# Performance work log

Hardware: AMD Instinct MI355X
Metric: run time of the kernel (lower is better)

## Reference

```python
import jax, jax.numpy as jnp
import numpy as np

# H2RConfig constants
KERNEL = 3
MAX_ROUTES = 1000
STRIDE = 4.0
MIN_SIZE = 32.0
MAX_SIZE = 512.0
SCORE_POWER = 2.0
UNC_WEIGHT = 0.35


def setup_inputs() -> dict:
    key = jax.random.key(0)
    k1, k2, k3 = jax.random.split(key, 3)
    shape = (32, 1, 512, 512)  # [B, 1, H, W] heatmaps at stride 4
    return {
        "route_logits": jax.random.normal(k1, shape, jnp.float32),
        "scale_logits": jax.random.normal(k2, shape, jnp.float32),
        "uncertainty_logits": jax.random.normal(k3, shape, jnp.float32),
        "image_h": 2048,
        "image_w": 2048,
    }


def reference(route_logits, scale_logits, uncertainty_logits, image_h, image_w):
    # score map: sigmoid^power, modulated by uncertainty (use_route_uncertainty=True)
    score = jnp.power(jax.nn.sigmoid(route_logits), SCORE_POWER)
    score = score * (1.0 - UNC_WEIGHT * jax.nn.sigmoid(uncertainty_logits))

    # local-max NMS: 3x3 max pool, stride 1, SAME padding (torch pads with -inf)
    pooled = jax.lax.reduce_window(
        score, -jnp.inf, jax.lax.max,
        window_dimensions=(1, 1, KERNEL, KERNEL),
        window_strides=(1, 1, 1, 1),
        padding="SAME",
    )
    peak_mask = score == pooled
    filtered = jnp.where(peak_mask, score, -1.0)

    B = score.shape[0]
    Wd = score.shape[3]
    flat = filtered.reshape(B, -1)                 # [B, H*W]
    values, indices = jax.lax.top_k(flat, MAX_ROUTES)  # [B, K]
    valid = values > 0.0                            # torch drops these; we mask/pad

    ys = indices // Wd
    xs = indices % Wd
    cx = (xs.astype(jnp.float32) + 0.5) * STRIDE
    cy = (ys.astype(jnp.float32) + 0.5) * STRIDE

    # gather scale / uncertainty at peak locations
    sc = jnp.take_along_axis(scale_logits.reshape(B, -1), indices, axis=1)
    un = jax.nn.sigmoid(jnp.take_along_axis(uncertainty_logits.reshape(B, -1), indices, axis=1))

    side = MIN_SIZE + jax.nn.sigmoid(sc) * (MAX_SIZE - MIN_SIZE)
    side = side * (1.0 + 0.25 * un)
    half = side * 0.5

    iw = float(image_w)
    ih = float(image_h)
    x1 = jnp.clip(cx - half, 0.0, iw - 1.0)
    y1 = jnp.clip(cy - half, 0.0, ih - 1.0)
    x2 = jnp.clip(cx + half, 1.0, iw)
    y2 = jnp.clip(cy + half, 1.0, ih)

    bcol = jnp.broadcast_to(jnp.arange(B, dtype=jnp.float32)[:, None], values.shape)
    rois = jnp.stack([bcol, x1, y1, x2, y2], axis=-1)  # [B, K, 5]

    # padded (fixed-shape) equivalent of torch's variable-length concat
    rois = jnp.where(valid[..., None], rois, 0.0)
    scores = jnp.where(valid, values, 0.0)
    return rois, scores, valid
```

## Files before the change

### kernel.cpp

```cpp
#include <hip/hip_runtime.h>
#include <hip/hip_bf16.h>
#include <math.h>


#define B_   32
#define H_   512
#define W_   512
#define HW_  (H_ * W_)
#define K_   1000
#define ROWS_ 16
#define THR_  512
#define PBUF_ 2048
#define PCAP_ 32768
#define CAND_ 2048

__device__ __forceinline__ float np_expf(float x) {
#pragma clang fp contract(off)
    const float log2e = 1.44269504088896341f;
    float z = x * log2e;
    float m = rintf(z);
    float r = fmaf(m, -0.693359375f, x);
    r = fmaf(m, 2.12194440e-4f, r);
    float r2 = r * r;
    float p = fmaf(1.9875691500e-4f, r, 1.3981999507e-3f);
    p = fmaf(p, r, 8.3334519073e-3f);
    p = fmaf(p, r, 4.1665795894e-2f);
    p = fmaf(p, r, 1.6666665459e-1f);
    p = fmaf(p, r, 5.0000001201e-1f);
    p = fmaf(p, r2, r);
    p = p + 1.0f;
    int mi = (int)m;
    float sc = __int_as_float((127 + mi) << 23);
    return p * sc;
}

__device__ __forceinline__ float sigmoid_np(float x) {
#pragma clang fp contract(off)
    float e = np_expf(-x);
    float d = 1.0f + e;
    return 1.0f / d;
}

__device__ __forceinline__ float score_ref(float r, float u) {
#pragma clang fp contract(off)
    float s  = sigmoid_np(r);
    float s2 = s * s;
    float su = sigmoid_np(u);
    float t  = 0.35f * su;
    float m  = 1.0f - t;
    return s2 * m;
}

__device__ __forceinline__ float sigmoid_fast(float x) {
    return 1.0f / (1.0f + __expf(-x));
}

__global__ __launch_bounds__(THR_, 4) void fused_peak_kernel(
    const float* __restrict__ route, const float* __restrict__ unc,
    unsigned long long* __restrict__ plist, int* __restrict__ peak_cnt)
{
    __shared__ float sm[ROWS_ + 2][W_];
    __shared__ unsigned long long pbuf[PBUF_];
    __shared__ int lcnt, gbase;

    const int tid   = threadIdx.x;
    const int strip = blockIdx.x;
    const int b     = blockIdx.y;
    const int r0    = strip * ROWS_;
    if (tid == 0) lcnt = 0;

    const float4* rb4 = (const float4*)(route + (size_t)b * HW_);
    const float4* ub4 = (const float4*)(unc   + (size_t)b * HW_);

    float4 rv[5], uv[5];
    int lrow[5], c4[5]; bool ok[5], act[5];
    #pragma unroll
    for (int k = 0; k < 5; ++k) {
        int slot = tid + k * THR_;
        act[k]  = slot < (ROWS_ + 2) * 128;
        int row = slot >> 7;
        int gy  = r0 - 1 + row;
        lrow[k] = row; c4[k] = slot & 127;
        ok[k]   = (gy >= 0 && gy < H_);
        int cy  = gy < 0 ? 0 : (gy >= H_ ? H_ - 1 : gy);
        if (act[k]) {
            rv[k] = rb4[cy * 128 + c4[k]];
            uv[k] = ub4[cy * 128 + c4[k]];
        }
    }
    #pragma unroll
    for (int k = 0; k < 5; ++k) {
        if (!act[k]) continue;
        float4 s;
        s.x = score_ref(rv[k].x, uv[k].x);
        s.y = score_ref(rv[k].y, uv[k].y);
        s.z = score_ref(rv[k].z, uv[k].z);
        s.w = score_ref(rv[k].w, uv[k].w);
        if (!ok[k]) { s.x = -INFINITY; s.y = -INFINITY;
                      s.z = -INFINITY; s.w = -INFINITY; }
        *(float4*)&sm[lrow[k]][c4[k] * 4] = s;
    }
    __syncthreads();

    #pragma unroll
    for (int j = 0; j < 4; ++j) {
        int g  = tid + j * THR_;
        int ly = 1 + (g >> 7);
        int x0 = (g & 127) * 4;
        int gy = r0 + (ly - 1);
        float w[3][6];
        #pragma unroll
        for (int r = 0; r < 3; ++r) {
            int rr = ly - 1 + r;
            w[r][0] = (x0 > 0) ? sm[rr][x0 - 1] : -INFINITY;
            w[r][1] = sm[rr][x0];
            w[r][2] = sm[rr][x0 + 1];
            w[r][3] = sm[rr][x0 + 2];
            w[r][4] = sm[rr][x0 + 3];
            w[r][5] = (x0 + 4 < W_) ? sm[rr][x0 + 4] : -INFINITY;
        }
        #pragma unroll
        for (int i = 0; i < 4; ++i) {
            float v = w[1][i + 1];
            float m = fmaxf(fmaxf(fmaxf(w[0][i], w[0][i + 1]),
                                  fmaxf(w[0][i + 2], w[1][i])),
                            fmaxf(fmaxf(w[1][i + 2], w[2][i]),
                                  fmaxf(w[2][i + 1], w[2][i + 2])));
            if (v >= m) {
                unsigned int bits = __float_as_uint(v);
                unsigned int idx  = (unsigned int)(gy * W_ + x0 + i);
                int p = atomicAdd(&lcnt, 1);
                if (p < PBUF_)
                    pbuf[p] = ((unsigned long long)bits << 32)
                              | (0xFFFFFFFFu - idx);
            }
        }
    }
    __syncthreads();
    if (tid == 0) {
        int n = lcnt < PBUF_ ? lcnt : PBUF_;
        gbase = atomicAdd(&peak_cnt[b], n);
    }
    __syncthreads();
    int n = lcnt < PBUF_ ? lcnt : PBUF_;
    int base = gbase;
    for (int i = tid; i < n; i += THR_) {
        int dst = base + i;
        if (dst < PCAP_) plist[(size_t)b * PCAP_ + dst] = pbuf[i];
    }
}

__global__ __launch_bounds__(1024) void select_kernel(
    const float* __restrict__ scale, const float* __restrict__ unc,
    const unsigned long long* __restrict__ plist,
    const int* __restrict__ peak_cnt,
    const int* __restrict__ ih_p, const int* __restrict__ iw_p,
    float* __restrict__ out)
{
    __shared__ unsigned int h16[8192];
    __shared__ unsigned long long cand[CAND_];
    __shared__ unsigned int ssum[1024];
    __shared__ int warp_s[16];
    __shared__ int sh_sum, sh_T, sh_n;

    const int b = blockIdx.x, tid = threadIdx.x;
    const int lane = tid & 63, wid = tid >> 6;
    if (tid == 0) { sh_T = 0; sh_n = 0; }
    for (int i = tid; i < 8192; i += 1024) h16[i] = 0u;
    __syncthreads();

    int pc = peak_cnt[b]; if (pc > PCAP_) pc = PCAP_;
    const unsigned long long* pl = plist + (size_t)b * PCAP_;

    for (int i = tid; i < pc; i += 1024) {
        unsigned int bits = (unsigned int)(pl[i] >> 32);
        unsigned int bkt  = bits >> 18;
        atomicAdd(&h16[bkt >> 1], 1u << ((bkt & 1) * 16));
    }
    __syncthreads();

    int total = 0;
    for (int c = 15; c >= 0; --c) {
        int bucket = c * 1024 + tid;
        unsigned int cnt = (h16[bucket >> 1] >> ((bucket & 1) * 16)) & 0xFFFFu;
        int v = (int)cnt;
        #pragma unroll
        for (int off = 32; off > 0; off >>= 1) v += __shfl_down(v, off, 64);
        if (lane == 0) warp_s[wid] = v;
        __syncthreads();
        if (tid == 0) {
            int s = 0;
            #pragma unroll
            for (int w = 0; w < 16; ++w) s += warp_s[w];
            sh_sum = s;
        }
        __syncthreads();
        int s = sh_sum;
        __syncthreads();
        if (total + s < K_) { total += s; continue; }
        ssum[tid] = cnt;
        __syncthreads();
        for (int off = 1; off < 1024; off <<= 1) {
            unsigned int vv = (tid + off < 1024) ? ssum[tid + off] : 0u;
            __syncthreads();
            ssum[tid] += vv;
            __syncthreads();
        }
        bool cond  = (total + (int)ssum[tid]) >= K_;
        bool cnext = (tid == 1023) ? false
                     : ((total + (int)ssum[tid + 1]) >= K_);
        if (cond && !cnext) sh_T = c * 1024 + tid;
        __syncthreads();
        break;
    }
    const unsigned int T = (unsigned int)sh_T;

    for (int i = tid; i < pc; i += 1024) {
        unsigned long long key = pl[i];
        if ((((unsigned int)(key >> 32)) >> 18) >= T) {
            int p = atomicAdd(&sh_n, 1);
            if (p < CAND_) cand[p] = key;
        }
    }
    __syncthreads();
    int nc = sh_n; if (nc > CAND_) nc = CAND_;
    for (int i = tid; i < CAND_; i += 1024)
        if (i >= nc) cand[i] = 0ull;

    for (int kk = 2; kk <= CAND_; kk <<= 1) {
        for (int jj = kk >> 1; jj > 0; jj >>= 1) {
            __syncthreads();
            for (int i = tid; i < CAND_; i += 1024) {
                int ixj = i ^ jj;
                if (ixj > i) {
                    bool desc = ((i & kk) == 0);
                    unsigned long long a = cand[i], c2 = cand[ixj];
                    if (desc ? (a < c2) : (a > c2)) { cand[i] = c2; cand[ixj] = a; }
                }
            }
        }
    }
    __syncthreads();

    const float fih = (float)(*ih_p);
    const float fiw = (float)(*iw_p);
    float* rois   = out;
    float* scores = out + (size_t)B_ * K_ * 5;
    float* validf = out + (size_t)B_ * K_ * 6;

    for (int k = tid; k < K_; k += 1024) {
        int o = b * K_ + k;
        unsigned long long key = cand[k];
        unsigned int bits = (unsigned int)(key >> 32);
        if (bits == 0u) {
            rois[o * 5 + 0] = 0.0f; rois[o * 5 + 1] = 0.0f;
            rois[o * 5 + 2] = 0.0f; rois[o * 5 + 3] = 0.0f;
            rois[o * 5 + 4] = 0.0f;
            scores[o] = 0.0f; validf[o] = 0.0f;
        } else {
            float v = __uint_as_float(bits);
            unsigned int idx = 0xFFFFFFFFu - (unsigned int)(key & 0xFFFFFFFFull);
            int y = (int)(idx >> 9), x = (int)(idx & 511u);
            float cx = ((float)x + 0.5f) * 4.0f;
            float cy = ((float)y + 0.5f) * 4.0f;
            float ss = sigmoid_fast(scale[(size_t)b * HW_ + idx]);
            float su = sigmoid_fast(unc  [(size_t)b * HW_ + idx]);
            float side = (32.0f + ss * 480.0f) * (1.0f + 0.25f * su);
            float half = 0.5f * side;
            float x1 = fminf(fmaxf(cx - half, 0.0f), fiw - 1.0f);
            float y1 = fminf(fmaxf(cy - half, 0.0f), fih - 1.0f);
            float x2 = fminf(fmaxf(cx + half, 1.0f), fiw);
            float y2 = fminf(fmaxf(cy + half, 1.0f), fih);
            rois[o * 5 + 0] = (float)b;
            rois[o * 5 + 1] = x1; rois[o * 5 + 2] = y1;
            rois[o * 5 + 3] = x2; rois[o * 5 + 4] = y2;
            scores[o] = v; validf[o] = 1.0f;
        }
    }
}

extern "C" void kernel_launch(void* const* d_in, const int* in_sizes, int n_in,
                              void* d_out, int out_size, void* d_ws, size_t ws_size,
                              hipStream_t stream) {
    const float* route = (const float*)d_in[0];
    const float* scale = (const float*)d_in[1];
    const float* unc   = (const float*)d_in[2];
    const int*   ih    = (const int*)d_in[3];
    const int*   iw    = (const int*)d_in[4];
    float* out = (float*)d_out;

    char* ws = (char*)d_ws;
    int* peak_cnt = (int*)ws;
    unsigned long long* plist = (unsigned long long*)(ws + 512);

    hipMemsetAsync(d_ws, 0, 512, stream);

    dim3 g(H_ / ROWS_, B_);
    fused_peak_kernel<<<g, THR_, 0, stream>>>(route, unc, plist, peak_cnt);
    select_kernel<<<B_, 1024, 0, stream>>>(scale, unc, plist, peak_cnt,
                                           ih, iw, out);
}
```

Baseline: 186.6 us.

## Refine top-k threshold with two-level histogram and shrink bitonic sort

The 3x3 max-pool now uses vectorised float4 shared-memory loads and separable column maxima instead of scalar loads and nine-way comparisons. In the select kernel, the coarse 16K-bucket histogram with block-wide scans becomes a 4K-bucket histogram scanned by a single wavefront with shuffles and ballot. A second-level histogram inside the threshold bucket runs when too many candidates would pass. Fewer candidates allow a 1024-element bitonic sort with compact pair indexing, at the cost of an extra pass over the peak list when refinement triggers.

```diff
diff --git a/kernel.cpp b/kernel.cpp
--- a/kernel.cpp
+++ b/kernel.cpp
@@ -13,6 +13,7 @@
 #define PBUF_ 2048
 #define PCAP_ 32768
 #define CAND_ 2048
+#define NBUK_ 4096
 
 __device__ __forceinline__ float np_expf(float x) {
 #pragma clang fp contract(off)
@@ -108,26 +109,36 @@
         int ly = 1 + (g >> 7);
         int x0 = (g & 127) * 4;
         int gy = r0 + (ly - 1);
-        float w[3][6];
-        #pragma unroll
-        for (int r = 0; r < 3; ++r) {
-            int rr = ly - 1 + r;
-            w[r][0] = (x0 > 0) ? sm[rr][x0 - 1] : -INFINITY;
-            w[r][1] = sm[rr][x0];
-            w[r][2] = sm[rr][x0 + 1];
-            w[r][3] = sm[rr][x0 + 2];
-            w[r][4] = sm[rr][x0 + 3];
-            w[r][5] = (x0 + 4 < W_) ? sm[rr][x0 + 4] : -INFINITY;
-        }
+        float4 q0 = *(const float4*)&sm[ly - 1][x0];
+        float4 q1 = *(const float4*)&sm[ly    ][x0];
+        float4 q2 = *(const float4*)&sm[ly + 1][x0];
+        bool hasL = (x0 > 0), hasR = (x0 + 4 < W_);
+        float l0 = hasL ? sm[ly - 1][x0 - 1] : -INFINITY;
+        float l1 = hasL ? sm[ly    ][x0 - 1] : -INFINITY;
+        float l2 = hasL ? sm[ly + 1][x0 - 1] : -INFINITY;
+        float e0 = hasR ? sm[ly - 1][x0 + 4] : -INFINITY;
+        float e1 = hasR ? sm[ly    ][x0 + 4] : -INFINITY;
+        float e2 = hasR ? sm[ly + 1][x0 + 4] : -INFINITY;
+        float f_m1 = fmaxf(l0, fmaxf(l1, l2));
+        float f_0  = fmaxf(q0.x, fmaxf(q1.x, q2.x));
+        float f_1  = fmaxf(q0.y, fmaxf(q1.y, q2.y));
+        float f_2  = fmaxf(q0.z, fmaxf(q1.z, q2.z));
+        float f_3  = fmaxf(q0.w, fmaxf(q1.w, q2.w));
+        float f_4  = fmaxf(e0, fmaxf(e1, e2));
+        float tb0  = fmaxf(q0.x, q2.x);
+        float tb1  = fmaxf(q0.y, q2.y);
+        float tb2  = fmaxf(q0.z, q2.z);
+        float tb3  = fmaxf(q0.w, q2.w);
+        float vv[4] = { q1.x, q1.y, q1.z, q1.w };
+        float mm[4];
+        mm[0] = fmaxf(fmaxf(f_m1, f_1), tb0);
+        mm[1] = fmaxf(fmaxf(f_0,  f_2), tb1);
+        mm[2] = fmaxf(fmaxf(f_1,  f_3), tb2);
+        mm[3] = fmaxf(fmaxf(f_2,  f_4), tb3);
         #pragma unroll
         for (int i = 0; i < 4; ++i) {
-            float v = w[1][i + 1];
-            float m = fmaxf(fmaxf(fmaxf(w[0][i], w[0][i + 1]),
-                                  fmaxf(w[0][i + 2], w[1][i])),
-                            fmaxf(fmaxf(w[1][i + 2], w[2][i]),
-                                  fmaxf(w[2][i + 1], w[2][i + 2])));
-            if (v >= m) {
-                unsigned int bits = __float_as_uint(v);
+            if (vv[i] >= mm[i]) {
+                unsigned int bits = __float_as_uint(vv[i]);
                 unsigned int idx  = (unsigned int)(gy * W_ + x0 + i);
                 int p = atomicAdd(&lcnt, 1);
                 if (p < PBUF_)
@@ -157,86 +168,124 @@
     const int* __restrict__ ih_p, const int* __restrict__ iw_p,
     float* __restrict__ out)
 {
-    __shared__ unsigned int h16[8192];
+    __shared__ unsigned int h16[NBUK_ / 2];
     __shared__ unsigned long long cand[CAND_];
-    __shared__ unsigned int ssum[1024];
-    __shared__ int warp_s[16];
-    __shared__ int sh_sum, sh_T, sh_n;
+    __shared__ int sh_T, sh_T2, sh_ref, sh_n;
 
     const int b = blockIdx.x, tid = threadIdx.x;
     const int lane = tid & 63, wid = tid >> 6;
-    if (tid == 0) { sh_T = 0; sh_n = 0; }
-    for (int i = tid; i < 8192; i += 1024) h16[i] = 0u;
+    if (tid == 0) { sh_T = 0; sh_T2 = 0; sh_ref = 0; sh_n = 0; }
+    for (int i = tid; i < NBUK_ / 2; i += 1024) h16[i] = 0u;
     __syncthreads();
 
     int pc = peak_cnt[b]; if (pc > PCAP_) pc = PCAP_;
     const unsigned long long* pl = plist + (size_t)b * PCAP_;
 
     for (int i = tid; i < pc; i += 1024) {
-        unsigned int bits = (unsigned int)(pl[i] >> 32);
-        unsigned int bkt  = bits >> 18;
+        unsigned int bkt = ((unsigned int)(pl[i] >> 32)) >> 18;
         atomicAdd(&h16[bkt >> 1], 1u << ((bkt & 1) * 16));
     }
     __syncthreads();
 
-    int total = 0;
-    for (int c = 15; c >= 0; --c) {
-        int bucket = c * 1024 + tid;
-        unsigned int cnt = (h16[bucket >> 1] >> ((bucket & 1) * 16)) & 0xFFFFu;
-        int v = (int)cnt;
-        #pragma unroll
-        for (int off = 32; off > 0; off >>= 1) v += __shfl_down(v, off, 64);
-        if (lane == 0) warp_s[wid] = v;
+    if (wid == 0) {
+        int total = 0;
+        for (int c = NBUK_ / 64 - 1; c >= 0; --c) {
+            int bucket = c * 64 + lane;
+            int cnt = (int)((h16[bucket >> 1] >> ((bucket & 1) * 16)) & 0xFFFFu);
+            int s = cnt;
+            #pragma unroll
+            for (int off = 32; off > 0; off >>= 1) s += __shfl_down(s, off, 64);
+            s = __shfl(s, 0, 64);
+            if (total + s < K_) { total += s; continue; }
+            int suf = cnt;
+            #pragma unroll
+            for (int off = 1; off < 64; off <<= 1) {
+                int o = __shfl_down(suf, off, 64);
+                suf += (lane + off < 64) ? o : 0;
+            }
+            bool cond = (total + suf) >= K_;
+            unsigned long long mask = __ballot(cond);
+            int ls = 63 - __builtin_clzll(mask);
+            int sufs = __shfl(suf, ls, 64);
+            int cnts = __shfl(cnt, ls, 64);
+            if (lane == 0) {
+                sh_T = c * 64 + ls;
+                int A = total + sufs - cnts;
+                sh_ref = (A + cnts > 1024) ? (0x40000000 | A) : 0;
+            }
+            break;
+        }
+    }
+    __syncthreads();
+    const unsigned int T = (unsigned int)sh_T;
+    const int refflag = sh_ref;
+    const int refined = (refflag >> 30) & 1;
+    const int A = refflag & 0x3FFFFFFF;
+
+    if (refined) {
+        for (int i = tid; i < NBUK_ / 2; i += 1024) h16[i] = 0u;
         __syncthreads();
-        if (tid == 0) {
-            int s = 0;
-            #pragma unroll
-            for (int w = 0; w < 16; ++w) s += warp_s[w];
-            sh_sum = s;
+        for (int i = tid; i < pc; i += 1024) {
+            unsigned int bits = (unsigned int)(pl[i] >> 32);
+            if ((bits >> 18) == T) {
+                unsigned int sb = (bits >> 6) & 0xFFFu;
+                atomicAdd(&h16[sb >> 1], 1u << ((sb & 1) * 16));
+            }
         }
         __syncthreads();
-        int s = sh_sum;
+        if (wid == 0) {
+            int total = A;
+            for (int c = NBUK_ / 64 - 1; c >= 0; --c) {
+                int bucket = c * 64 + lane;
+                int cnt = (int)((h16[bucket >> 1] >> ((bucket & 1) * 16)) & 0xFFFFu);
+                int s = cnt;
+                #pragma unroll
+                for (int off = 32; off > 0; off >>= 1) s += __shfl_down(s, off, 64);
+                s = __shfl(s, 0, 64);
+                if (total + s < K_) { total += s; continue; }
+                int suf = cnt;
+                #pragma unroll
+                for (int off = 1; off < 64; off <<= 1) {
+                    int o = __shfl_down(suf, off, 64);
+                    suf += (lane + off < 64) ? o : 0;
+                }
+                bool cond = (total + suf) >= K_;
+                unsigned long long mask = __ballot(cond);
+                int ls = 63 - __builtin_clzll(mask);
+                if (lane == 0) sh_T2 = c * 64 + ls;
+                break;
+            }
+        }
         __syncthreads();
-        if (total + s < K_) { total += s; continue; }
-        ssum[tid] = cnt;
-        __syncthreads();
-        for (int off = 1; off < 1024; off <<= 1) {
-            unsigned int vv = (tid + off < 1024) ? ssum[tid + off] : 0u;
-            __syncthreads();
-            ssum[tid] += vv;
-            __syncthreads();
-        }
-        bool cond  = (total + (int)ssum[tid]) >= K_;
-        bool cnext = (tid == 1023) ? false
-                     : ((total + (int)ssum[tid + 1]) >= K_);
-        if (cond && !cnext) sh_T = c * 1024 + tid;
-        __syncthreads();
-        break;
-    }
-    const unsigned int T = (unsigned int)sh_T;
+    }
+    const unsigned int T2 = (unsigned int)sh_T2;
 
     for (int i = tid; i < pc; i += 1024) {
         unsigned long long key = pl[i];
-        if ((((unsigned int)(key >> 32)) >> 18) >= T) {
+        unsigned int bits = (unsigned int)(key >> 32);
+        unsigned int bkt  = bits >> 18;
+        bool take = (bkt > T) ||
+                    (bkt == T && (!refined || (((bits >> 6) & 0xFFFu) >= T2)));
+        if (take) {
             int p = atomicAdd(&sh_n, 1);
             if (p < CAND_) cand[p] = key;
         }
     }
     __syncthreads();
     int nc = sh_n; if (nc > CAND_) nc = CAND_;
-    for (int i = tid; i < CAND_; i += 1024)
+    int sortN = (nc <= 1024) ? 1024 : CAND_;
+    for (int i = tid; i < sortN; i += 1024)
         if (i >= nc) cand[i] = 0ull;
 
-    for (int kk = 2; kk <= CAND_; kk <<= 1) {
+    for (int kk = 2; kk <= sortN; kk <<= 1) {
         for (int jj = kk >> 1; jj > 0; jj >>= 1) {
             __syncthreads();
-            for (int i = tid; i < CAND_; i += 1024) {
-                int ixj = i ^ jj;
-                if (ixj > i) {
-                    bool desc = ((i & kk) == 0);
-                    unsigned long long a = cand[i], c2 = cand[ixj];
-                    if (desc ? (a < c2) : (a > c2)) { cand[i] = c2; cand[ixj] = a; }
-                }
+            for (int p = tid; p < (sortN >> 1); p += 1024) {
+                int i   = ((p & ~(jj - 1)) << 1) | (p & (jj - 1));
+                int ixj = i | jj;
+                bool desc = ((i & kk) == 0);
+                unsigned long long a = cand[i], c2 = cand[ixj];
+                if (desc ? (a < c2) : (a > c2)) { cand[i] = c2; cand[ixj] = a; }
             }
         }
     }
```

Measured after the change: 181.0 us. 3.0% less time.
